# Optimization experiments

Measured on AMD Instinct MI355X. Metric: run time of the kernel, lower is better.

Reference implementation:

```python
import jax, jax.numpy as jnp
from jax import lax
import numpy as np

B, C, T = 256, 64, 4096   # batch, in_channels, seq_len
H, K, NBLK, O = 64, 2, 4, 64  # hidden_channels, kernel, blocks, out_channels


def _conv1d(x, w, b, stride=1):
    # x: [N,C,T], w: [Cout,Cin,K], b: [Cout]
    y = lax.conv_general_dilated(x, w, window_strides=(stride,), padding='VALID',
                                 dimension_numbers=('NCH', 'OIH', 'NCH'))
    return y + b[None, :, None]


def setup_inputs() -> dict:
    key = jax.random.key(0)
    ks = jax.random.split(key, 12)
    s = 0.05  # small init so relu/sigmoid stay in sane range across 4 blocks
    return {
        'x': jax.random.normal(ks[0], (B, C, T), jnp.float32),
        'sig_w': jax.random.normal(ks[1], (NBLK, H, C, K), jnp.float32) * s,
        'sig_b': jax.random.normal(ks[2], (NBLK, H), jnp.float32) * s,
        'gate_w': jax.random.normal(ks[3], (NBLK, H, C, K), jnp.float32) * s,
        'gate_b': jax.random.normal(ks[4], (NBLK, H), jnp.float32) * s,
        'out_w': jax.random.normal(ks[5], (NBLK, C, H, 1), jnp.float32) * s,
        'out_b': jax.random.normal(ks[6], (NBLK, C), jnp.float32) * s,
        'skip_w': jax.random.normal(ks[7], (O, C, 1), jnp.float32) * s,
        'skip_b': jax.random.normal(ks[8], (O,), jnp.float32) * s,
        'dil_w': jax.random.normal(ks[9], (C, C, 2), jnp.float32) * s,
        'dil_b': jax.random.normal(ks[10], (C,), jnp.float32) * s,
    }


def reference(x, sig_w, sig_b, gate_w, gate_b, out_w, out_b,
              skip_w, skip_b, dil_w, dil_b):
    kk = sig_w.shape[-1]
    g = x
    for i in range(sig_w.shape[0]):  # fixed small number of blocks
        padded = jnp.pad(g, ((0, 0), (0, 0), (kk - 1, 0)))  # causal left-pad
        s = jax.nn.relu(_conv1d(padded, sig_w[i], sig_b[i]))
        gt = jax.nn.sigmoid(_conv1d(padded, gate_w[i], gate_b[i]))
        g = g + _conv1d(s * gt, out_w[i], out_b[i])  # 1x1 conv + residual
    dilated = _conv1d(jnp.pad(g, ((0, 0), (0, 0), (1, 0))), dil_w, dil_b, stride=2)
    skip = _conv1d(g[:, :, -1:], skip_w, skip_b)  # 1x1 conv on last step
    return dilated, skip
```

## Files before the change

### kernel.cpp

```cpp
#include <hip/hip_runtime.h>

typedef short s16x8 __attribute__((ext_vector_type(8)));
typedef short s16x4 __attribute__((ext_vector_type(4)));
typedef float f32x4 __attribute__((ext_vector_type(4)));

#define CH 64
#define TSEQ 4096
#define TOUT 2048
#define NBLK 4
#define COLS 112
#define TT 106
#define HALO 6
#define NTILE 39
#define NT 7
#define GBROW 72
#define QPT 53
#define DIL_TOTAL 33554432

#define WA_OFF 0
#define WO_OFF 131072
#define WD_OFF 163840
#define SK_BYTE_OFF 360448

__device__ __forceinline__ short f2bf(float x) {
  unsigned u = __float_as_uint(x);
  return (short)((u + 0x7fffu + ((u >> 16) & 1u)) >> 16);
}
__device__ __forceinline__ float bf2f(short h) {
  return __uint_as_float(((unsigned)(unsigned short)h) << 16);
}
__device__ __forceinline__ f32x4 mfma16(s16x8 a, s16x8 b, f32x4 c) {
  return __builtin_amdgcn_mfma_f32_16x16x32_bf16(a, b, c, 0, 0, 0);
}

__global__ void prep(const float* __restrict__ sig_w, const float* __restrict__ gate_w,
                     const float* __restrict__ out_w, const float* __restrict__ dil_w,
                     const float* __restrict__ skip_w, short* __restrict__ wsS,
                     float* __restrict__ wsF) {
  const int idx = blockIdx.x * 256 + threadIdx.x;
  if (idx < 131072) {
    const int inner = idx & 2047, grp = idx >> 11;
    const int tap = grp & 1, kc = (grp >> 1) & 1, half = (grp >> 2) & 1;
    const int mat = (grp >> 3) & 1, blk = grp >> 4;
    const int h = inner >> 5, c = kc * 32 + (inner & 31);
    const float* W = mat ? gate_w : sig_w;
    const float w = W[((blk * CH + h) * CH + c) * 2 + tap];
    const short hi = f2bf(w);
    wsS[WA_OFF + idx] = half ? f2bf(w - bf2f(hi)) : hi;
  } else if (idx < 163840) {
    const int i2 = idx - 131072;
    const int inner = i2 & 2047, grp = i2 >> 11;
    const int kc = grp & 1, half = (grp >> 1) & 1, blk = grp >> 2;
    const int c = inner >> 5, h = kc * 32 + (inner & 31);
    const float w = out_w[(blk * CH + c) * CH + h];
    const short hi = f2bf(w);
    wsS[idx] = half ? f2bf(w - bf2f(hi)) : hi;
  } else if (idx < 180224) {
    const int i3 = idx - 163840;
    const int inner = i3 & 2047, grp = i3 >> 11;
    const int tap = grp & 1, kc = (grp >> 1) & 1, half = (grp >> 2) & 1;
    const int co = inner >> 5, ci = kc * 32 + (inner & 31);
    const float w = dil_w[(co * CH + ci) * 2 + tap];
    const short hi = f2bf(w);
    wsS[idx] = half ? f2bf(w - bf2f(hi)) : hi;
  } else if (idx < 184320) {
    const int i4 = idx - 180224;
    const int ci = i4 >> 6, o = i4 & 63;
    wsF[i4] = skip_w[o * CH + ci];
  }
}

__global__ __launch_bounds__(256, 3)
void wavenet_mfma(const float* __restrict__ x,
                  const float* __restrict__ sig_b, const float* __restrict__ gate_b,
                  const float* __restrict__ out_b, const float* __restrict__ skip_b,
                  const float* __restrict__ dil_b, const short* __restrict__ wsS,
                  const float* __restrict__ wsF, float* __restrict__ out) {
  __shared__ __align__(16) short GBs[2 * 113 * GBROW];
  __shared__ __align__(16) short GEs[113 * GBROW];

  const int tile = blockIdx.x % NTILE;
  const int b    = blockIdx.x / NTILE;
  const int t0   = tile * TT;
  const int tid  = threadIdx.x;
  const int lane = tid & 63;
  const int wv   = tid >> 6;
  const int n    = lane & 15;
  const int g4   = lane >> 4;
  const int hbase = wv * 16;
  const int cch  = hbase + g4 * 4;

  for (int idx = tid; idx < CH * COLS; idx += 256) {
    const int c = idx / COLS, p = idx - c * COLS;
    const int tg = t0 - HALO + p;
    float v = 0.f;
    if (tg >= 0 && tg < TSEQ) v = x[(b * CH + c) * TSEQ + tg];
    const short hi = f2bf(v);
    const float lf = v - bf2f(hi);
    const short lo = f2bf(lf);
    GBs[(p + 1) * GBROW + c] = hi;
    GBs[(113 + p + 1) * GBROW + c] = lo;
    GEs[(p + 1) * GBROW + c] = f2bf(lf - bf2f(lo));
  }
  if (tid < 2 * GBROW) {
    const int half = tid / GBROW;
    GBs[half * 113 * GBROW + (tid - half * GBROW)] = 0;
  } else if (tid < 3 * GBROW) {
    GEs[tid - 2 * GBROW] = 0;
  }
  __syncthreads();

  const short* bpH0 = &GBs[(n + 0) * GBROW + g4 * 8];
  const short* bpH1 = &GBs[(n + 1) * GBROW + g4 * 8];
  const short* bpL0 = &GBs[(113 + n + 0) * GBROW + g4 * 8];
  const short* bpL1 = &GBs[(113 + n + 1) * GBROW + g4 * 8];
  const int lo_p = (tile == 0) ? HALO : 0;
  const int lbase = (hbase + n) * 32 + g4 * 8;

#pragma unroll 1
  for (int blk = 0; blk < NBLK; ++blk) {
    s16x8 wS[2][2][2], wG[2][2][2];
#pragma unroll
    for (int half = 0; half < 2; ++half)
#pragma unroll
      for (int kc = 0; kc < 2; ++kc)
#pragma unroll
        for (int tap = 0; tap < 2; ++tap) {
          wS[half][kc][tap] = *(const s16x8*)&wsS[WA_OFF + ((((blk*2+0)*2+half)*2+kc)*2+tap)*2048 + lbase];
          wG[half][kc][tap] = *(const s16x8*)&wsS[WA_OFF + ((((blk*2+1)*2+half)*2+kc)*2+tap)*2048 + lbase];
        }

    f32x4 aS[NT], aG[NT];
#pragma unroll
    for (int j = 0; j < NT; ++j) { aS[j] = (f32x4)0.f; aG[j] = (f32x4)0.f; }
#pragma unroll
    for (int j = 0; j < NT; ++j) {
      const int ro = j * 16 * GBROW;
#pragma unroll
      for (int kc = 0; kc < 2; ++kc) {
        const int co = ro + kc * 32;
        {
          const s16x8 bh = *(const s16x8*)(bpH0 + co);
          const s16x8 bl = *(const s16x8*)(bpL0 + co);
          aS[j] = mfma16(wS[0][kc][0], bh, aS[j]);
          aS[j] = mfma16(wS[1][kc][0], bh, aS[j]);
          aS[j] = mfma16(wS[0][kc][0], bl, aS[j]);
          aG[j] = mfma16(wG[0][kc][0], bh, aG[j]);
          aG[j] = mfma16(wG[1][kc][0], bh, aG[j]);
          aG[j] = mfma16(wG[0][kc][0], bl, aG[j]);
        }
        {
          const s16x8 bh = *(const s16x8*)(bpH1 + co);
          const s16x8 bl = *(const s16x8*)(bpL1 + co);
          aS[j] = mfma16(wS[0][kc][1], bh, aS[j]);
          aS[j] = mfma16(wS[1][kc][1], bh, aS[j]);
          aS[j] = mfma16(wS[0][kc][1], bl, aS[j]);
          aG[j] = mfma16(wG[0][kc][1], bh, aG[j]);
          aG[j] = mfma16(wG[1][kc][1], bh, aG[j]);
          aG[j] = mfma16(wG[0][kc][1], bl, aG[j]);
        }
      }
    }
    __syncthreads();

    f32x4 gOld[NT];
    const f32x4 bs4 = *(const f32x4*)(sig_b  + blk * 64 + cch);
    const f32x4 bg4 = *(const f32x4*)(gate_b + blk * 64 + cch);
#pragma unroll
    for (int j = 0; j < NT; ++j) {
      const int r1 = j * 16 + n + 1;
      const s16x4 oh = *(const s16x4*)&GBs[r1 * GBROW + cch];
      const s16x4 ol = *(const s16x4*)&GBs[(113 + r1) * GBROW + cch];
      const s16x4 oe = *(const s16x4*)&GEs[r1 * GBROW + cch];
      s16x4 uh, ul;
#pragma unroll
      for (int r = 0; r < 4; ++r) {
        gOld[j][r] = bf2f(oh[r]) + bf2f(ol[r]) + bf2f(oe[r]);
        const float s = fmaxf(aS[j][r] + bs4[r], 0.f);
        const float t = aG[j][r] + bg4[r];
        const float u = s * __builtin_amdgcn_rcpf(1.f + __expf(-t));
        const short hi = f2bf(u);
        uh[r] = hi; ul[r] = f2bf(u - bf2f(hi));
      }
      *(s16x4*)&GBs[r1 * GBROW + cch] = uh;
      *(s16x4*)&GBs[(113 + r1) * GBROW + cch] = ul;
    }
    __syncthreads();

    s16x8 wO2[2][2];
#pragma unroll
    for (int half = 0; half < 2; ++half)
#pragma unroll
      for (int kc = 0; kc < 2; ++kc)
        wO2[half][kc] = *(const s16x8*)&wsS[WO_OFF + ((blk*2+half)*2+kc)*2048 + lbase];
    f32x4 aO[NT];
    const f32x4 ob4 = *(const f32x4*)(out_b + blk * 64 + cch);
#pragma unroll
    for (int j = 0; j < NT; ++j) aO[j] = ob4;
#pragma unroll
    for (int j = 0; j < NT; ++j) {
      const int ro = j * 16 * GBROW;
#pragma unroll
      for (int kc = 0; kc < 2; ++kc) {
        const s16x8 uh = *(const s16x8*)(bpH1 + ro + kc * 32);
        const s16x8 ul = *(const s16x8*)(bpL1 + ro + kc * 32);
        aO[j] = mfma16(wO2[0][kc], uh, aO[j]);
        aO[j] = mfma16(wO2[1][kc], uh, aO[j]);
        aO[j] = mfma16(wO2[0][kc], ul, aO[j]);
      }
    }
    __syncthreads();

#pragma unroll
    for (int j = 0; j < NT; ++j) {
      const int p = j * 16 + n;
      const f32x4 nv = (p >= lo_p) ? (f32x4)(gOld[j] + aO[j]) : gOld[j];
      s16x4 nh, nl, ne;
#pragma unroll
      for (int r = 0; r < 4; ++r) {
        const short hi = f2bf(nv[r]);
        const float lf = nv[r] - bf2f(hi);
        const short lo = f2bf(lf);
        nh[r] = hi; nl[r] = lo; ne[r] = f2bf(lf - bf2f(lo));
      }
      *(s16x4*)&GBs[(p + 1) * GBROW + cch] = nh;
      *(s16x4*)&GBs[(113 + p + 1) * GBROW + cch] = nl;
      *(s16x4*)&GEs[(p + 1) * GBROW + cch] = ne;
    }
    __syncthreads();
  }

  {
    s16x8 wD[2][2][2];
#pragma unroll
    for (int half = 0; half < 2; ++half)
#pragma unroll
      for (int kc = 0; kc < 2; ++kc)
#pragma unroll
        for (int tap = 0; tap < 2; ++tap)
          wD[half][kc][tap] = *(const s16x8*)&wsS[WD_OFF + ((half*2+kc)*2+tap)*2048 + lbase];
    const f32x4 db4 = *(const f32x4*)(dil_b + cch);
    const int tau0 = tile * QPT;
#pragma unroll
    for (int j = 0; j < 4; ++j) {
      const int idx = j * 16 + n;
      const int idxc = (idx < QPT) ? idx : (QPT - 1);
      f32x4 ad = db4;
      const int rbase = (6 + idxc * 2) * GBROW + g4 * 8;
#pragma unroll
      for (int kc = 0; kc < 2; ++kc)
#pragma unroll
        for (int tap = 0; tap < 2; ++tap) {
          const s16x8 bh = *(const s16x8*)&GBs[rbase + tap * GBROW + kc * 32];
          const s16x8 bl = *(const s16x8*)&GBs[113 * GBROW + rbase + tap * GBROW + kc * 32];
          ad = mfma16(wD[0][kc][tap], bh, ad);
          ad = mfma16(wD[1][kc][tap], bh, ad);
          ad = mfma16(wD[0][kc][tap], bl, ad);
        }
      const int tau = tau0 + idx;
      if (idx < QPT && tau < TOUT) {
        const int cobase = b * CH + cch;
#pragma unroll
        for (int r = 0; r < 4; ++r)
          out[(cobase + r) * TOUT + tau] = ad[r];
      }
    }
  }

  if (tile == NTILE - 1 && wv == 0) {
    const int o = lane;
    float a = skip_b[o];
    for (int c = 0; c < CH; ++c) {
      const float g = bf2f(GBs[74 * GBROW + c]) + bf2f(GBs[(113 + 74) * GBROW + c])
                    + bf2f(GEs[74 * GBROW + c]);
      a = fmaf(wsF[c * CH + o], g, a);
    }
    out[DIL_TOTAL + b * CH + o] = a;
  }
}

extern "C" void kernel_launch(void* const* d_in, const int* in_sizes, int n_in,
                              void* d_out, int out_size, void* d_ws, size_t ws_size,
                              hipStream_t stream) {
  const float* x      = (const float*)d_in[0];
  const float* sig_w  = (const float*)d_in[1];
  const float* sig_b  = (const float*)d_in[2];
  const float* gate_w = (const float*)d_in[3];
  const float* gate_b = (const float*)d_in[4];
  const float* out_w  = (const float*)d_in[5];
  const float* out_b  = (const float*)d_in[6];
  const float* skip_w = (const float*)d_in[7];
  const float* skip_b = (const float*)d_in[8];
  const float* dil_w  = (const float*)d_in[9];
  const float* dil_b  = (const float*)d_in[10];
  short* wsS = (short*)d_ws;
  float* wsF = (float*)((char*)d_ws + SK_BYTE_OFF);
  float* out = (float*)d_out;

  prep<<<dim3(720), dim3(256), 0, stream>>>(sig_w, gate_w, out_w, dil_w, skip_w, wsS, wsF);
  wavenet_mfma<<<dim3(256 * NTILE), dim3(256), 0, stream>>>(
      x, sig_b, gate_b, out_b, skip_b, dil_b, (const short*)wsS, (const float*)wsF, out);
}
```

Measured before the change: 1.116 ms.

## Drop third residual split, truncate bf16 splits, loop over k-chunks to cut registers

```diff
diff --git a/kernel.cpp b/kernel.cpp
--- a/kernel.cpp
+++ b/kernel.cpp
@@ -25,6 +25,9 @@
 __device__ __forceinline__ short f2bf(float x) {
   unsigned u = __float_as_uint(x);
   return (short)((u + 0x7fffu + ((u >> 16) & 1u)) >> 16);
+}
+__device__ __forceinline__ short f2bf_tr(float x) {
+  return (short)(__float_as_uint(x) >> 16);
 }
 __device__ __forceinline__ float bf2f(short h) {
   return __uint_as_float(((unsigned)(unsigned short)h) << 16);
@@ -70,14 +73,13 @@
   }
 }
 
-__global__ __launch_bounds__(256, 3)
+__global__ __launch_bounds__(256, 4)
 void wavenet_mfma(const float* __restrict__ x,
                   const float* __restrict__ sig_b, const float* __restrict__ gate_b,
                   const float* __restrict__ out_b, const float* __restrict__ skip_b,
                   const float* __restrict__ dil_b, const short* __restrict__ wsS,
                   const float* __restrict__ wsF, float* __restrict__ out) {
   __shared__ __align__(16) short GBs[2 * 113 * GBROW];
-  __shared__ __align__(16) short GEs[113 * GBROW];
 
   const int tile = blockIdx.x % NTILE;
   const int b    = blockIdx.x / NTILE;
@@ -95,70 +97,45 @@
     const int tg = t0 - HALO + p;
     float v = 0.f;
     if (tg >= 0 && tg < TSEQ) v = x[(b * CH + c) * TSEQ + tg];
-    const short hi = f2bf(v);
-    const float lf = v - bf2f(hi);
-    const short lo = f2bf(lf);
+    const short hi = f2bf_tr(v);
     GBs[(p + 1) * GBROW + c] = hi;
-    GBs[(113 + p + 1) * GBROW + c] = lo;
-    GEs[(p + 1) * GBROW + c] = f2bf(lf - bf2f(lo));
+    GBs[(113 + p + 1) * GBROW + c] = f2bf_tr(v - bf2f(hi));
   }
   if (tid < 2 * GBROW) {
     const int half = tid / GBROW;
     GBs[half * 113 * GBROW + (tid - half * GBROW)] = 0;
-  } else if (tid < 3 * GBROW) {
-    GEs[tid - 2 * GBROW] = 0;
   }
   __syncthreads();
 
-  const short* bpH0 = &GBs[(n + 0) * GBROW + g4 * 8];
-  const short* bpH1 = &GBs[(n + 1) * GBROW + g4 * 8];
-  const short* bpL0 = &GBs[(113 + n + 0) * GBROW + g4 * 8];
-  const short* bpL1 = &GBs[(113 + n + 1) * GBROW + g4 * 8];
   const int lo_p = (tile == 0) ? HALO : 0;
   const int lbase = (hbase + n) * 32 + g4 * 8;
 
 #pragma unroll 1
   for (int blk = 0; blk < NBLK; ++blk) {
-    s16x8 wS[2][2][2], wG[2][2][2];
-#pragma unroll
-    for (int half = 0; half < 2; ++half)
-#pragma unroll
-      for (int kc = 0; kc < 2; ++kc)
-#pragma unroll
-        for (int tap = 0; tap < 2; ++tap) {
-          wS[half][kc][tap] = *(const s16x8*)&wsS[WA_OFF + ((((blk*2+0)*2+half)*2+kc)*2+tap)*2048 + lbase];
-          wG[half][kc][tap] = *(const s16x8*)&wsS[WA_OFF + ((((blk*2+1)*2+half)*2+kc)*2+tap)*2048 + lbase];
-        }
-
     f32x4 aS[NT], aG[NT];
 #pragma unroll
     for (int j = 0; j < NT; ++j) { aS[j] = (f32x4)0.f; aG[j] = (f32x4)0.f; }
-#pragma unroll
-    for (int j = 0; j < NT; ++j) {
-      const int ro = j * 16 * GBROW;
-#pragma unroll
-      for (int kc = 0; kc < 2; ++kc) {
-        const int co = ro + kc * 32;
-        {
-          const s16x8 bh = *(const s16x8*)(bpH0 + co);
-          const s16x8 bl = *(const s16x8*)(bpL0 + co);
-          aS[j] = mfma16(wS[0][kc][0], bh, aS[j]);
-          aS[j] = mfma16(wS[1][kc][0], bh, aS[j]);
-          aS[j] = mfma16(wS[0][kc][0], bl, aS[j]);
-          aG[j] = mfma16(wG[0][kc][0], bh, aG[j]);
-          aG[j] = mfma16(wG[1][kc][0], bh, aG[j]);
-          aG[j] = mfma16(wG[0][kc][0], bl, aG[j]);
-        }
-        {
-          const s16x8 bh = *(const s16x8*)(bpH1 + co);
-          const s16x8 bl = *(const s16x8*)(bpL1 + co);
-          aS[j] = mfma16(wS[0][kc][1], bh, aS[j]);
-          aS[j] = mfma16(wS[1][kc][1], bh, aS[j]);
-          aS[j] = mfma16(wS[0][kc][1], bl, aS[j]);
-          aG[j] = mfma16(wG[0][kc][1], bh, aG[j]);
-          aG[j] = mfma16(wG[1][kc][1], bh, aG[j]);
-          aG[j] = mfma16(wG[0][kc][1], bl, aG[j]);
-        }
+#pragma unroll 1
+    for (int kt = 0; kt < 4; ++kt) {
+      const int kc = kt >> 1, tap = kt & 1;
+      const int wa = WA_OFF + blk * 32768 + kc * 4096 + tap * 2048 + lbase;
+      const s16x8 wS0 = *(const s16x8*)&wsS[wa];
+      const s16x8 wS1 = *(const s16x8*)&wsS[wa + 8192];
+      const s16x8 wG0 = *(const s16x8*)&wsS[wa + 16384];
+      const s16x8 wG1 = *(const s16x8*)&wsS[wa + 16384 + 8192];
+      const short* bH = &GBs[(n + tap) * GBROW + g4 * 8 + kc * 32];
+      const short* bL = bH + 113 * GBROW;
+#pragma unroll
+      for (int j = 0; j < NT; ++j) {
+        const int ro = j * 16 * GBROW;
+        const s16x8 bh = *(const s16x8*)(bH + ro);
+        const s16x8 bl = *(const s16x8*)(bL + ro);
+        aS[j] = mfma16(wS0, bh, aS[j]);
+        aS[j] = mfma16(wS1, bh, aS[j]);
+        aS[j] = mfma16(wS0, bl, aS[j]);
+        aG[j] = mfma16(wG0, bh, aG[j]);
+        aG[j] = mfma16(wG1, bh, aG[j]);
+        aG[j] = mfma16(wG0, bl, aG[j]);
       }
     }
     __syncthreads();
@@ -171,42 +148,40 @@
       const int r1 = j * 16 + n + 1;
       const s16x4 oh = *(const s16x4*)&GBs[r1 * GBROW + cch];
       const s16x4 ol = *(const s16x4*)&GBs[(113 + r1) * GBROW + cch];
-      const s16x4 oe = *(const s16x4*)&GEs[r1 * GBROW + cch];
       s16x4 uh, ul;
 #pragma unroll
       for (int r = 0; r < 4; ++r) {
-        gOld[j][r] = bf2f(oh[r]) + bf2f(ol[r]) + bf2f(oe[r]);
+        gOld[j][r] = bf2f(oh[r]) + bf2f(ol[r]);
         const float s = fmaxf(aS[j][r] + bs4[r], 0.f);
         const float t = aG[j][r] + bg4[r];
         const float u = s * __builtin_amdgcn_rcpf(1.f + __expf(-t));
-        const short hi = f2bf(u);
-        uh[r] = hi; ul[r] = f2bf(u - bf2f(hi));
+        const short hi = f2bf_tr(u);
+        uh[r] = hi; ul[r] = f2bf_tr(u - bf2f(hi));
       }
       *(s16x4*)&GBs[r1 * GBROW + cch] = uh;
       *(s16x4*)&GBs[(113 + r1) * GBROW + cch] = ul;
     }
     __syncthreads();
 
-    s16x8 wO2[2][2];
-#pragma unroll
-    for (int half = 0; half < 2; ++half)
-#pragma unroll
-      for (int kc = 0; kc < 2; ++kc)
-        wO2[half][kc] = *(const s16x8*)&wsS[WO_OFF + ((blk*2+half)*2+kc)*2048 + lbase];
     f32x4 aO[NT];
     const f32x4 ob4 = *(const f32x4*)(out_b + blk * 64 + cch);
 #pragma unroll
     for (int j = 0; j < NT; ++j) aO[j] = ob4;
-#pragma unroll
-    for (int j = 0; j < NT; ++j) {
-      const int ro = j * 16 * GBROW;
-#pragma unroll
-      for (int kc = 0; kc < 2; ++kc) {
-        const s16x8 uh = *(const s16x8*)(bpH1 + ro + kc * 32);
-        const s16x8 ul = *(const s16x8*)(bpL1 + ro + kc * 32);
-        aO[j] = mfma16(wO2[0][kc], uh, aO[j]);
-        aO[j] = mfma16(wO2[1][kc], uh, aO[j]);
-        aO[j] = mfma16(wO2[0][kc], ul, aO[j]);
+#pragma unroll 1
+    for (int kc = 0; kc < 2; ++kc) {
+      const int wo = WO_OFF + blk * 8192 + kc * 2048 + lbase;
+      const s16x8 wO0 = *(const s16x8*)&wsS[wo];
+      const s16x8 wO1 = *(const s16x8*)&wsS[wo + 4096];
+      const short* uH = &GBs[(n + 1) * GBROW + g4 * 8 + kc * 32];
+      const short* uL = uH + 113 * GBROW;
+#pragma unroll
+      for (int j = 0; j < NT; ++j) {
+        const int ro = j * 16 * GBROW;
+        const s16x8 uh = *(const s16x8*)(uH + ro);
+        const s16x8 ul = *(const s16x8*)(uL + ro);
+        aO[j] = mfma16(wO0, uh, aO[j]);
+        aO[j] = mfma16(wO1, uh, aO[j]);
+        aO[j] = mfma16(wO0, ul, aO[j]);
       }
     }
     __syncthreads();
@@ -215,17 +190,14 @@
     for (int j = 0; j < NT; ++j) {
       const int p = j * 16 + n;
       const f32x4 nv = (p >= lo_p) ? (f32x4)(gOld[j] + aO[j]) : gOld[j];
-      s16x4 nh, nl, ne;
+      s16x4 nh, nl;
 #pragma unroll
       for (int r = 0; r < 4; ++r) {
-        const short hi = f2bf(nv[r]);
-        const float lf = nv[r] - bf2f(hi);
-        const short lo = f2bf(lf);
-        nh[r] = hi; nl[r] = lo; ne[r] = f2bf(lf - bf2f(lo));
+        const short hi = f2bf_tr(nv[r]);
+        nh[r] = hi; nl[r] = f2bf_tr(nv[r] - bf2f(hi));
       }
       *(s16x4*)&GBs[(p + 1) * GBROW + cch] = nh;
       *(s16x4*)&GBs[(113 + p + 1) * GBROW + cch] = nl;
-      *(s16x4*)&GEs[(p + 1) * GBROW + cch] = ne;
     }
     __syncthreads();
   }
@@ -271,8 +243,7 @@
     const int o = lane;
     float a = skip_b[o];
     for (int c = 0; c < CH; ++c) {
-      const float g = bf2f(GBs[74 * GBROW + c]) + bf2f(GBs[(113 + 74) * GBROW + c])
-                    + bf2f(GEs[74 * GBROW + c]);
+      const float g = bf2f(GBs[74 * GBROW + c]) + bf2f(GBs[(113 + 74) * GBROW + c]);
       a = fmaf(wsF[c * CH + o], g, a);
     }
     out[DIL_TOTAL + b * CH + o] = a;
```

Measured after the change: 967.6 us. -13.3%, faster.
